# Kernel tuning notes

Hardware: AMD Instinct MI355X
Metric: run time of the kernel (lower is better)

## Reference

```python
import jax, jax.numpy as jnp
import numpy as np
import math

B, S, DM, H = 4, 2048, 1024, 16
HD = DM // H

def setup_inputs() -> dict:
    key = jax.random.key(0)
    ks = jax.random.split(key, 12)
    def lin(k, din, dout):
        bound = 1.0 / math.sqrt(din)
        kw, kb = jax.random.split(k)
        W = jax.random.uniform(kw, (din, dout), jnp.float32, -bound, bound)
        b = jax.random.uniform(kb, (dout,), jnp.float32, -bound, bound)
        return W, b
    Wq, bq = lin(ks[0], DM, DM)
    Wk, bk = lin(ks[1], DM, DM)
    Wv, bv = lin(ks[2], DM, DM)
    Wo, bo = lin(ks[3], DM, DM)
    return {
        "Q": jax.random.normal(ks[4], (B, S, DM), jnp.float32),
        "K": jax.random.normal(ks[5], (B, S, DM), jnp.float32),
        "V": jax.random.normal(ks[6], (B, S, DM), jnp.float32),
        "mask": jnp.ones((B, S), jnp.int32),
        "Wq": Wq, "bq": bq, "Wk": Wk, "bk": bk,
        "Wv": Wv, "bv": bv, "Wo": Wo, "bo": bo,
    }

def reference(Q, K, V, mask, Wq, bq, Wk, bk, Wv, bv, Wo, bo):
    N, qlen, dm = Q.shape
    klen = K.shape[1]
    q = (Q @ Wq + bq).reshape(N, qlen, H, HD)
    k = (K @ Wk + bk).reshape(N, klen, H, HD)
    v = (V @ Wv + bv).reshape(N, klen, H, HD)
    # scores: [B, q, H, k]
    dot = jnp.einsum('bqhd,bkhd->bqhk', q, k) / math.sqrt(HD)
    # mask is 2-D (N, klen): broadcast as (N, 1, 1, klen); positions where mask==0 are masked
    m = (mask == 0)[:, None, None, :]
    dot = jnp.where(m, -jnp.inf, dot)
    weights = jax.nn.softmax(dot.astype(jnp.float32), axis=-1).astype(dot.dtype)
    out = jnp.einsum('bqhk,bkhd->bqhd', weights, v).reshape(N, qlen, dm)
    return out @ Wo + bo
```

## Files before the change

kernel.cpp:

```cpp
#include <hip/hip_runtime.h>
#include <math.h>

#define B_  4
#define S_  2048
#define DM_ 1024
#define H_  16
#define HD_ 64

typedef float f32x4 __attribute__((ext_vector_type(4)));
typedef short bf16x8 __attribute__((ext_vector_type(8)));

#define MFMA16(a, b, c) __builtin_amdgcn_mfma_f32_16x16x32_bf16((a), (b), (c), 0, 0, 0)

static __device__ __forceinline__ unsigned short f2bf(float f) {
    union { float f; unsigned int i; } c; c.f = f;
    unsigned int u = c.i;
    return (unsigned short)((u + 0x7fffu + ((u >> 16) & 1u)) >> 16);
}
static __device__ __forceinline__ unsigned int f2u(float f) {
    union { float f; unsigned int u; } c; c.f = f; return c.u;
}

static __device__ __forceinline__ void async16(const void* g, void* l) {
    __builtin_amdgcn_global_load_lds(
        (__attribute__((address_space(1))) void*)(void*)g,
        (__attribute__((address_space(3))) void*)l, 16, 0, 0);
}

__global__ __launch_bounds__(256) void prep_all(
    const float* __restrict__ Q, const float* __restrict__ K,
    const float* __restrict__ V, const int* __restrict__ mask,
    const float* __restrict__ w0, const float* __restrict__ w1,
    const float* __restrict__ w2, const float* __restrict__ w3,
    unsigned short* __restrict__ qo, unsigned short* __restrict__ ko,
    unsigned short* __restrict__ vo,
    unsigned short* __restrict__ o0, unsigned short* __restrict__ o1,
    unsigned short* __restrict__ o2, unsigned short* __restrict__ o3,
    float* __restrict__ maddf, unsigned int* __restrict__ flags)
{
    __shared__ float tile[64][65];
    const int id = blockIdx.x, t = threadIdx.x;
    if (id < 12288) {
        const int z = id >> 12, x = id & 4095;
        const float* in = z == 0 ? Q : (z == 1 ? K : V);
        unsigned short* out = z == 0 ? qo : (z == 1 ? ko : vo);
        int idx = (x * 256 + t) * 8;
        float4 a = *(const float4*)(in + idx);
        float4 b = *(const float4*)(in + idx + 4);
        *(ushort4*)(out + idx)     = make_ushort4(f2bf(a.x), f2bf(a.y), f2bf(a.z), f2bf(a.w));
        *(ushort4*)(out + idx + 4) = make_ushort4(f2bf(b.x), f2bf(b.y), f2bf(b.z), f2bf(b.w));
    } else if (id < 13312) {
        const int rr = id - 12288;
        const int z = rr >> 8, ky = (rr >> 4) & 15, nx = rr & 15;
        const float* W = z == 0 ? w0 : (z == 1 ? w1 : (z == 2 ? w2 : w3));
        unsigned short* Wt = z == 0 ? o0 : (z == 1 ? o1 : (z == 2 ? o2 : o3));
        const int k0 = ky * 64, n0 = nx * 64;
        const int r = t >> 4, c4 = (t & 15) * 4;
        #pragma unroll
        for (int s = 0; s < 4; ++s) {
            float4 f = *(const float4*)(W + (size_t)(k0 + s * 16 + r) * DM_ + n0 + c4);
            tile[s * 16 + r][c4 + 0] = f.x; tile[s * 16 + r][c4 + 1] = f.y;
            tile[s * 16 + r][c4 + 2] = f.z; tile[s * 16 + r][c4 + 3] = f.w;
        }
        __syncthreads();
        #pragma unroll
        for (int s = 0; s < 4; ++s) {
            int n = s * 16 + r;
            ushort4 o = make_ushort4(f2bf(tile[c4 + 0][n]), f2bf(tile[c4 + 1][n]),
                                     f2bf(tile[c4 + 2][n]), f2bf(tile[c4 + 3][n]));
            *(ushort4*)(Wt + (size_t)(n0 + n) * DM_ + k0 + c4) = o;
        }
    } else {
        int i = (id - 13312) * 256 + t;
        int m = mask[i];
        maddf[i] = m ? 0.f : -__builtin_inff();
        unsigned long long bal = __ballot(m != 0);
        if ((t & 63) == 0)
            flags[i >> 6] = (bal == 0xFFFFFFFFFFFFFFFFull) ? 1u : 0u;
    }
}

static __device__ __forceinline__ void gemm_body(
    const unsigned short* __restrict__ A,
    const unsigned short* __restrict__ Wt,
    const float* __restrict__ bias,
    void* __restrict__ outp, int mode, float oscale, int m0, int n0,
    unsigned short (*As)[128 * 64], unsigned short (*Bs)[128 * 64])
{
    const int t = threadIdx.x;
    const int w = t >> 6, l = t & 63;
    const int quad = l >> 4, l16 = l & 15;
    const int wr = w >> 1, wc = w & 1;

    const int srow8 = l >> 3;
    const int sch   = (l & 7) ^ srow8;
    const unsigned short* ag = A  + (size_t)(m0 + w * 32 + srow8) * DM_ + sch * 8;
    const unsigned short* bg = Wt + (size_t)(n0 + w * 32 + srow8) * DM_ + sch * 8;

    const f32x4 fz = {0.f, 0.f, 0.f, 0.f};
    f32x4 acc[4][4];
    #pragma unroll
    for (int i = 0; i < 4; ++i)
        #pragma unroll
        for (int j = 0; j < 4; ++j) acc[i][j] = fz;

    const int rsw = l16 & 7;

    auto stageAB = [&](int d, int k0) {
        #pragma unroll
        for (int s = 0; s < 4; ++s) {
            async16(ag + k0 + (size_t)(s * 8) * DM_, &As[d][(w * 32 + s * 8) * 64]);
            async16(bg + k0 + (size_t)(s * 8) * DM_, &Bs[d][(w * 32 + s * 8) * 64]);
        }
    };

    stageAB(0, 0);
    int cur = 0;
    for (int k0 = 0; k0 < DM_; k0 += 64) {
        __syncthreads();
        if (k0 + 64 < DM_) stageAB(cur ^ 1, k0 + 64);
        #pragma unroll
        for (int c = 0; c < 2; ++c) {
            const int csw = ((c * 4 + quad) ^ rsw) * 8;
            bf16x8 af[4], bfr[4];
            #pragma unroll
            for (int i = 0; i < 4; ++i)
                af[i] = *(const bf16x8*)&As[cur][(wr * 64 + i * 16 + l16) * 64 + csw];
            #pragma unroll
            for (int j = 0; j < 4; ++j)
                bfr[j] = *(const bf16x8*)&Bs[cur][(wc * 64 + j * 16 + l16) * 64 + csw];
            #pragma unroll
            for (int i = 0; i < 4; ++i)
                #pragma unroll
                for (int j = 0; j < 4; ++j)
                    acc[i][j] = MFMA16(af[i], bfr[j], acc[i][j]);
        }
        cur ^= 1;
    }

    float bv[4];
    #pragma unroll
    for (int j = 0; j < 4; ++j) bv[j] = bias[n0 + wc * 64 + j * 16 + l16];

    if (mode == 2) {
        float* out = (float*)outp;
        #pragma unroll
        for (int i = 0; i < 4; ++i)
            #pragma unroll
            for (int j = 0; j < 4; ++j) {
                int col = n0 + wc * 64 + j * 16 + l16;
                #pragma unroll
                for (int r = 0; r < 4; ++r) {
                    int row = m0 + wr * 64 + i * 16 + quad * 4 + r;
                    out[(size_t)row * DM_ + col] = acc[i][j][r] + bv[j];
                }
            }
    } else if (mode == 0) {
        unsigned short* out = (unsigned short*)outp;
        #pragma unroll
        for (int i = 0; i < 4; ++i)
            #pragma unroll
            for (int j = 0; j < 4; ++j) {
                int col = n0 + wc * 64 + j * 16 + l16;
                int h = col >> 6, d = col & 63;
                #pragma unroll
                for (int r = 0; r < 4; ++r) {
                    int row = m0 + wr * 64 + i * 16 + quad * 4 + r;
                    int bb = row >> 11, ss = row & (S_ - 1);
                    out[(((size_t)bb * H_ + h) * S_ + ss) * HD_ + d] =
                        f2bf((acc[i][j][r] + bv[j]) * oscale);
                }
            }
    } else {
        unsigned short* out = (unsigned short*)outp;
        #pragma unroll
        for (int i = 0; i < 4; ++i)
            #pragma unroll
            for (int j = 0; j < 4; ++j) {
                int col = n0 + wc * 64 + j * 16 + l16;
                int h = col >> 6, d = col & 63;
                int row0 = m0 + wr * 64 + i * 16 + quad * 4;
                int bb = row0 >> 11, ss = row0 & (S_ - 1);
                ushort4 o = make_ushort4(f2bf(acc[i][j][0] + bv[j]),
                                         f2bf(acc[i][j][1] + bv[j]),
                                         f2bf(acc[i][j][2] + bv[j]),
                                         f2bf(acc[i][j][3] + bv[j]));
                *(ushort4*)(out + (((size_t)bb * H_ + h) * HD_ + d) * S_ + ss) = o;
            }
    }
}

__global__ __launch_bounds__(256) void gemm_qkv3(
    const unsigned short* __restrict__ Qc, const unsigned short* __restrict__ Kc,
    const unsigned short* __restrict__ Vc,
    const unsigned short* __restrict__ Wqt, const unsigned short* __restrict__ Wkt,
    const unsigned short* __restrict__ Wvt,
    const float* __restrict__ bq, const float* __restrict__ bk,
    const float* __restrict__ bvp,
    unsigned short* __restrict__ qh, unsigned short* __restrict__ kh,
    unsigned short* __restrict__ vth)
{
    __shared__ unsigned short As[2][128 * 64];
    __shared__ unsigned short Bs[2][128 * 64];
    const int id = blockIdx.x;
    const int role = (id & 7) * 192 + (id >> 3);
    const int z = role >> 9, r2 = role & 511;
    const int m0 = (r2 >> 3) * 128, n0 = (r2 & 7) * 128;
    const unsigned short* A  = z == 0 ? Qc  : (z == 1 ? Kc  : Vc);
    const unsigned short* Wt = z == 0 ? Wqt : (z == 1 ? Wkt : Wvt);
    const float* bias        = z == 0 ? bq  : (z == 1 ? bk  : bvp);
    void* out                = z == 0 ? (void*)qh : (z == 1 ? (void*)kh : (void*)vth);
    const float qsc = 0.18033688011112042f;
    gemm_body(A, Wt, bias, out, z == 2 ? 1 : 0, z == 0 ? qsc : 1.0f, m0, n0, As, Bs);
}

__global__ __launch_bounds__(256) void gemm_omfma(
    const unsigned short* __restrict__ A, const unsigned short* __restrict__ Wt,
    const float* __restrict__ bias, float* __restrict__ out)
{
    __shared__ unsigned short As[2][128 * 64];
    __shared__ unsigned short Bs[2][128 * 64];
    const int id = blockIdx.x;
    const int role = (id & 7) * 64 + (id >> 3);
    const int m0 = (role >> 3) * 128, n0 = (role & 7) * 128;
    gemm_body(A, Wt, bias, out, 2, 1.0f, m0, n0, As, Bs);
}

template<bool MASKED>
static __device__ __forceinline__ void softmax_store(
    const f32x4* sc, const float (*madd)[4], unsigned short* Pg,
    int l16, int quad, int rsw)
{
    #pragma unroll
    for (int kk = 0; kk < 4; ++kk) {
        int kb = (kk * 2 + (quad >> 1)) ^ rsw;
        #pragma unroll
        for (int rp = 0; rp < 2; ++rp) {
            float a0 = sc[kk][rp * 2 + 0], a1 = sc[kk][rp * 2 + 1];
            if (MASKED) { a0 += madd[kk][rp * 2 + 0]; a1 += madd[kk][rp * 2 + 1]; }
            float p0 = __builtin_amdgcn_exp2f(a0);
            float p1 = __builtin_amdgcn_exp2f(a1);
            unsigned int pk = __builtin_amdgcn_perm(f2u(p1), f2u(p0), 0x07060302u);
            *(unsigned int*)&Pg[l16 * 64 + kb * 8 + (quad & 1) * 4 + rp * 2] = pk;
        }
    }
}

__global__ __launch_bounds__(256) void attn_mfma(
    const unsigned short* __restrict__ q,
    const unsigned short* __restrict__ k,
    const unsigned short* __restrict__ vt,
    const float* __restrict__ maddf,
    const unsigned int* __restrict__ flags,
    unsigned short* __restrict__ out)
{
    __shared__ unsigned short Ks[2][64 * 64];
    __shared__ unsigned short Vs[2][64 * 64];
    __shared__ unsigned short Ps[4][2][16 * 64];
    const int t = threadIdx.x;
    const int w = t >> 6, l = t & 63;
    const int quad = l >> 4, l16 = l & 15;

    const int bid = blockIdx.x;
    const int swz = (bid & 7) * 128 + (bid >> 3);
    const int qb = swz & 15, h = (swz >> 4) & 15, b = swz >> 8;
    const int q0 = qb * 128;
    const size_t hb = ((size_t)b * H_ + h) * S_;

    const int srow8 = l >> 3;
    const int sch   = (l & 7) ^ srow8;
    const int rsw   = l16 & 7;

    const unsigned short* qg = q + (hb + q0) * HD_;
    bf16x8 qf[2][2];
    #pragma unroll
    for (int g = 0; g < 2; ++g)
        #pragma unroll
        for (int c = 0; c < 2; ++c)
            qf[g][c] = *(const bf16x8*)(qg +
                (size_t)(w * 32 + g * 16 + l16) * HD_ + (c * 4 + quad) * 8);

    const bf16x8 onesf = {(short)0x3F80, (short)0x3F80, (short)0x3F80, (short)0x3F80,
                          (short)0x3F80, (short)0x3F80, (short)0x3F80, (short)0x3F80};

    const f32x4 fz = {0.f, 0.f, 0.f, 0.f};
    f32x4 o[2][4];
    f32x4 ol[2] = {fz, fz};
    #pragma unroll
    for (int g = 0; g < 2; ++g)
        #pragma unroll
        for (int jv = 0; jv < 4; ++jv) o[g][jv] = fz;

    const unsigned short* kg0 = k + hb * HD_;
    const unsigned short* vg0 = vt + ((size_t)b * H_ + h) * HD_ * S_;

    auto stage = [&](int d, int kt) {
        #pragma unroll
        for (int s = 0; s < 2; ++s) {
            int r0 = w * 16 + s * 8;
            int rr = r0 + srow8;
            async16(kg0 + (size_t)(kt * 64 + rr) * HD_ + sch * 8, &Ks[d][r0 * 64]);
            async16(vg0 + (size_t)rr * S_ + kt * 64 + sch * 8, &Vs[d][r0 * 64]);
        }
    };

    stage(0, 0);
    int cur = 0;
    for (int kt = 0; kt < S_ / 64; ++kt) {
        __syncthreads();
        if (kt + 1 < S_ / 64) stage(cur ^ 1, kt + 1);

        const int allv = flags[b * (S_ / 64) + kt];
        float madd[4][4];
        if (!allv) {
            #pragma unroll
            for (int kk = 0; kk < 4; ++kk) {
                float4 mv = *(const float4*)&maddf[(size_t)b * S_ + kt * 64 + kk * 16 + quad * 4];
                madd[kk][0] = mv.x; madd[kk][1] = mv.y;
                madd[kk][2] = mv.z; madd[kk][3] = mv.w;
            }
        }

        const unsigned short* Kc = &Ks[cur][0];
        bf16x8 kf[4][2];
        #pragma unroll
        for (int kk = 0; kk < 4; ++kk) {
            int row = kk * 16 + l16;
            #pragma unroll
            for (int c = 0; c < 2; ++c)
                kf[kk][c] = *(const bf16x8*)&Kc[row * 64 + (((c * 4 + quad) ^ rsw) * 8)];
        }
        #pragma unroll
        for (int g = 0; g < 2; ++g) {
            f32x4 sc[4];
            #pragma unroll
            for (int kk = 0; kk < 4; ++kk) sc[kk] = fz;
            __builtin_amdgcn_s_setprio(1);
            #pragma unroll
            for (int kk = 0; kk < 4; ++kk) {
                sc[kk] = MFMA16(kf[kk][0], qf[g][0], sc[kk]);
                sc[kk] = MFMA16(kf[kk][1], qf[g][1], sc[kk]);
            }
            __builtin_amdgcn_s_setprio(0);
            if (allv) softmax_store<false>(sc, madd, &Ps[w][g][0], l16, quad, rsw);
            else      softmax_store<true >(sc, madd, &Ps[w][g][0], l16, quad, rsw);
        }

        const unsigned short* Vc = &Vs[cur][0];
        bf16x8 vfr[4][2];
        #pragma unroll
        for (int jv = 0; jv < 4; ++jv) {
            int row = jv * 16 + l16;
            #pragma unroll
            for (int c = 0; c < 2; ++c)
                vfr[jv][c] = *(const bf16x8*)&Vc[row * 64 + (((c * 4 + quad) ^ rsw) * 8)];
        }
        #pragma unroll
        for (int g = 0; g < 2; ++g) {
            bf16x8 pa0 = *(const bf16x8*)&Ps[w][g][l16 * 64 + ((quad ^ rsw) * 8)];
            bf16x8 pa1 = *(const bf16x8*)&Ps[w][g][l16 * 64 + (((4 + quad) ^ rsw) * 8)];
            __builtin_amdgcn_s_setprio(1);
            #pragma unroll
            for (int jv = 0; jv < 4; ++jv) {
                o[g][jv] = MFMA16(pa0, vfr[jv][0], o[g][jv]);
                o[g][jv] = MFMA16(pa1, vfr[jv][1], o[g][jv]);
            }
            ol[g] = MFMA16(pa0, onesf, ol[g]);
            ol[g] = MFMA16(pa1, onesf, ol[g]);
            __builtin_amdgcn_s_setprio(0);
        }
        cur ^= 1;
    }

    #pragma unroll
    for (int g = 0; g < 2; ++g) {
        float inv[4];
        #pragma unroll
        for (int r = 0; r < 4; ++r) inv[r] = 1.0f / ol[g][r];
        #pragma unroll
        for (int jv = 0; jv < 4; ++jv) {
            int col = h * HD_ + jv * 16 + l16;
            #pragma unroll
            for (int r = 0; r < 4; ++r) {
                int row = q0 + w * 32 + g * 16 + quad * 4 + r;
                out[((size_t)b * S_ + row) * DM_ + col] = f2bf(o[g][jv][r] * inv[r]);
            }
        }
    }
}

extern "C" void kernel_launch(void* const* d_in, const int* in_sizes, int n_in,
                              void* d_out, int out_size, void* d_ws, size_t ws_size,
                              hipStream_t stream) {
    const float* Q    = (const float*)d_in[0];
    const float* K    = (const float*)d_in[1];
    const float* V    = (const float*)d_in[2];
    const int*   mask = (const int*)d_in[3];
    const float* Wq   = (const float*)d_in[4];
    const float* bq   = (const float*)d_in[5];
    const float* Wk   = (const float*)d_in[6];
    const float* bk   = (const float*)d_in[7];
    const float* Wv   = (const float*)d_in[8];
    const float* bv   = (const float*)d_in[9];
    const float* Wo   = (const float*)d_in[10];
    const float* bo   = (const float*)d_in[11];

    char* ws = (char*)d_ws;
    const size_t MB = 1024 * 1024;
    unsigned short* Qc  = (unsigned short*)(ws);
    unsigned short* Kc  = (unsigned short*)(ws + 16 * MB);
    unsigned short* Vc  = (unsigned short*)(ws + 32 * MB);
    unsigned short* Wqt = (unsigned short*)(ws + 48 * MB);
    unsigned short* Wkt = (unsigned short*)(ws + 50 * MB);
    unsigned short* Wvt = (unsigned short*)(ws + 52 * MB);
    unsigned short* Wot = (unsigned short*)(ws + 54 * MB);
    unsigned short* qh  = (unsigned short*)(ws + 56 * MB);
    unsigned short* kh  = (unsigned short*)(ws + 72 * MB);
    unsigned short* vth = (unsigned short*)(ws + 88 * MB);
    unsigned short* ao  = (unsigned short*)(ws + 104 * MB);
    float*          maddf = (float*)(ws + 120 * MB);
    unsigned int*   flagsb = (unsigned int*)(ws + 120 * MB + 64 * 1024);

    prep_all<<<dim3(13344), 256, 0, stream>>>(
        Q, K, V, mask, Wq, Wk, Wv, Wo,
        Qc, Kc, Vc, Wqt, Wkt, Wvt, Wot, maddf, flagsb);
    gemm_qkv3<<<dim3(1536), 256, 0, stream>>>(
        Qc, Kc, Vc, Wqt, Wkt, Wvt, bq, bk, bv, qh, kh, vth);
    attn_mfma<<<dim3(1024), 256, 0, stream>>>(
        qh, kh, vth, maddf, flagsb, ao);
    gemm_omfma<<<dim3(512), 256, 0, stream>>>(ao, Wot, bo, (float*)d_out);
}
```

Baseline: 342.6 us.

## Enlarge GEMM tiles to 256x128 and drop LDS double buffering

The shared GEMM body now computes 256x128 output tiles, with each wave holding 8x4 MFMA accumulators, instead of 128x128. The double-buffered LDS staging is replaced by a single buffer with load-then-sync each k-step, and grid sizes are halved. The goal is more reuse of the weight tile per block and fewer blocks. In exchange, loads no longer overlap compute, register pressure rises, and there are fewer blocks to spread across the CUs.

```diff
diff --git a/kernel.cpp b/kernel.cpp
--- a/kernel.cpp
+++ b/kernel.cpp
@@ -85,7 +85,7 @@
     const unsigned short* __restrict__ Wt,
     const float* __restrict__ bias,
     void* __restrict__ outp, int mode, float oscale, int m0, int n0,
-    unsigned short (*As)[128 * 64], unsigned short (*Bs)[128 * 64])
+    unsigned short* As, unsigned short* Bs)
 {
     const int t = threadIdx.x;
     const int w = t >> 6, l = t & 63;
@@ -94,48 +94,42 @@
 
     const int srow8 = l >> 3;
     const int sch   = (l & 7) ^ srow8;
-    const unsigned short* ag = A  + (size_t)(m0 + w * 32 + srow8) * DM_ + sch * 8;
+    const unsigned short* ag = A  + (size_t)(m0 + w * 64 + srow8) * DM_ + sch * 8;
     const unsigned short* bg = Wt + (size_t)(n0 + w * 32 + srow8) * DM_ + sch * 8;
 
     const f32x4 fz = {0.f, 0.f, 0.f, 0.f};
-    f32x4 acc[4][4];
-    #pragma unroll
-    for (int i = 0; i < 4; ++i)
+    f32x4 acc[8][4];
+    #pragma unroll
+    for (int i = 0; i < 8; ++i)
         #pragma unroll
         for (int j = 0; j < 4; ++j) acc[i][j] = fz;
 
     const int rsw = l16 & 7;
-
-    auto stageAB = [&](int d, int k0) {
-        #pragma unroll
-        for (int s = 0; s < 4; ++s) {
-            async16(ag + k0 + (size_t)(s * 8) * DM_, &As[d][(w * 32 + s * 8) * 64]);
-            async16(bg + k0 + (size_t)(s * 8) * DM_, &Bs[d][(w * 32 + s * 8) * 64]);
-        }
-    };
-
-    stageAB(0, 0);
-    int cur = 0;
     for (int k0 = 0; k0 < DM_; k0 += 64) {
         __syncthreads();
-        if (k0 + 64 < DM_) stageAB(cur ^ 1, k0 + 64);
+        #pragma unroll
+        for (int s = 0; s < 8; ++s)
+            async16(ag + k0 + (size_t)(s * 8) * DM_, &As[(w * 64 + s * 8) * 64]);
+        #pragma unroll
+        for (int s = 0; s < 4; ++s)
+            async16(bg + k0 + (size_t)(s * 8) * DM_, &Bs[(w * 32 + s * 8) * 64]);
+        __syncthreads();
         #pragma unroll
         for (int c = 0; c < 2; ++c) {
             const int csw = ((c * 4 + quad) ^ rsw) * 8;
-            bf16x8 af[4], bfr[4];
-            #pragma unroll
-            for (int i = 0; i < 4; ++i)
-                af[i] = *(const bf16x8*)&As[cur][(wr * 64 + i * 16 + l16) * 64 + csw];
+            bf16x8 af[8], bfr[4];
+            #pragma unroll
+            for (int i = 0; i < 8; ++i)
+                af[i] = *(const bf16x8*)&As[(wr * 128 + i * 16 + l16) * 64 + csw];
             #pragma unroll
             for (int j = 0; j < 4; ++j)
-                bfr[j] = *(const bf16x8*)&Bs[cur][(wc * 64 + j * 16 + l16) * 64 + csw];
-            #pragma unroll
-            for (int i = 0; i < 4; ++i)
+                bfr[j] = *(const bf16x8*)&Bs[(wc * 64 + j * 16 + l16) * 64 + csw];
+            #pragma unroll
+            for (int i = 0; i < 8; ++i)
                 #pragma unroll
                 for (int j = 0; j < 4; ++j)
                     acc[i][j] = MFMA16(af[i], bfr[j], acc[i][j]);
         }
-        cur ^= 1;
     }
 
     float bv[4];
@@ -145,27 +139,27 @@
     if (mode == 2) {
         float* out = (float*)outp;
         #pragma unroll
-        for (int i = 0; i < 4; ++i)
+        for (int i = 0; i < 8; ++i)
             #pragma unroll
             for (int j = 0; j < 4; ++j) {
                 int col = n0 + wc * 64 + j * 16 + l16;
                 #pragma unroll
                 for (int r = 0; r < 4; ++r) {
-                    int row = m0 + wr * 64 + i * 16 + quad * 4 + r;
+                    int row = m0 + wr * 128 + i * 16 + quad * 4 + r;
                     out[(size_t)row * DM_ + col] = acc[i][j][r] + bv[j];
                 }
             }
     } else if (mode == 0) {
         unsigned short* out = (unsigned short*)outp;
         #pragma unroll
-        for (int i = 0; i < 4; ++i)
+        for (int i = 0; i < 8; ++i)
             #pragma unroll
             for (int j = 0; j < 4; ++j) {
                 int col = n0 + wc * 64 + j * 16 + l16;
                 int h = col >> 6, d = col & 63;
                 #pragma unroll
                 for (int r = 0; r < 4; ++r) {
-                    int row = m0 + wr * 64 + i * 16 + quad * 4 + r;
+                    int row = m0 + wr * 128 + i * 16 + quad * 4 + r;
                     int bb = row >> 11, ss = row & (S_ - 1);
                     out[(((size_t)bb * H_ + h) * S_ + ss) * HD_ + d] =
                         f2bf((acc[i][j][r] + bv[j]) * oscale);
@@ -174,12 +168,12 @@
     } else {
         unsigned short* out = (unsigned short*)outp;
         #pragma unroll
-        for (int i = 0; i < 4; ++i)
+        for (int i = 0; i < 8; ++i)
             #pragma unroll
             for (int j = 0; j < 4; ++j) {
                 int col = n0 + wc * 64 + j * 16 + l16;
                 int h = col >> 6, d = col & 63;
-                int row0 = m0 + wr * 64 + i * 16 + quad * 4;
+                int row0 = m0 + wr * 128 + i * 16 + quad * 4;
                 int bb = row0 >> 11, ss = row0 & (S_ - 1);
                 ushort4 o = make_ushort4(f2bf(acc[i][j][0] + bv[j]),
                                          f2bf(acc[i][j][1] + bv[j]),
@@ -200,12 +194,12 @@
     unsigned short* __restrict__ qh, unsigned short* __restrict__ kh,
     unsigned short* __restrict__ vth)
 {
-    __shared__ unsigned short As[2][128 * 64];
-    __shared__ unsigned short Bs[2][128 * 64];
+    __shared__ unsigned short As[256 * 64];
+    __shared__ unsigned short Bs[128 * 64];
     const int id = blockIdx.x;
-    const int role = (id & 7) * 192 + (id >> 3);
-    const int z = role >> 9, r2 = role & 511;
-    const int m0 = (r2 >> 3) * 128, n0 = (r2 & 7) * 128;
+    const int role = (id & 7) * 96 + (id >> 3);
+    const int z = role >> 8, r2 = role & 255;
+    const int m0 = (r2 >> 3) * 256, n0 = (r2 & 7) * 128;
     const unsigned short* A  = z == 0 ? Qc  : (z == 1 ? Kc  : Vc);
     const unsigned short* Wt = z == 0 ? Wqt : (z == 1 ? Wkt : Wvt);
     const float* bias        = z == 0 ? bq  : (z == 1 ? bk  : bvp);
@@ -218,11 +212,11 @@
     const unsigned short* __restrict__ A, const unsigned short* __restrict__ Wt,
     const float* __restrict__ bias, float* __restrict__ out)
 {
-    __shared__ unsigned short As[2][128 * 64];
-    __shared__ unsigned short Bs[2][128 * 64];
+    __shared__ unsigned short As[256 * 64];
+    __shared__ unsigned short Bs[128 * 64];
     const int id = blockIdx.x;
-    const int role = (id & 7) * 64 + (id >> 3);
-    const int m0 = (role >> 3) * 128, n0 = (role & 7) * 128;
+    const int role = (id & 7) * 32 + (id >> 3);
+    const int m0 = (role >> 3) * 256, n0 = (role & 7) * 128;
     gemm_body(A, Wt, bias, out, 2, 1.0f, m0, n0, As, Bs);
 }
 
@@ -424,9 +418,9 @@
     prep_all<<<dim3(13344), 256, 0, stream>>>(
         Q, K, V, mask, Wq, Wk, Wv, Wo,
         Qc, Kc, Vc, Wqt, Wkt, Wvt, Wot, maddf, flagsb);
-    gemm_qkv3<<<dim3(1536), 256, 0, stream>>>(
+    gemm_qkv3<<<dim3(768), 256, 0, stream>>>(
         Qc, Kc, Vc, Wqt, Wkt, Wvt, bq, bk, bv, qh, kh, vth);
     attn_mfma<<<dim3(1024), 256, 0, stream>>>(
         qh, kh, vth, maddf, flagsb, ao);
-    gemm_omfma<<<dim3(512), 256, 0, stream>>>(ao, Wot, bo, (float*)d_out);
-}
+    gemm_omfma<<<dim3(256), 256, 0, stream>>>(ao, Wot, bo, (float*)d_out);
+}
```

Measured after the change: 385.7 us. 1.13x slower.
